# Kernel optimization log

Hardware: AMD Instinct MI355X
Metric: run time of the kernel (lower is better)

## Reference

```python
import jax, jax.numpy as jnp
import numpy as np

B, N, D, H = 8, 4096, 256, 4
KP, KN = N // 16, N // 32
EPS = 1e-6

def _ln(x, g, b):
    m = jnp.mean(x, -1, keepdims=True)
    v = jnp.var(x, -1, keepdims=True)
    return (x - m) / jnp.sqrt(v + 1e-5) * g + b

def _cross_attn(q_in, kv_in, wq, wk, wv, wo, bo):
    # q_in [1,Nq,D], kv_in [1,Nk,D]
    Bq, Nq, Dm = q_in.shape
    Nk = kv_in.shape[1]
    dh = Dm // H
    q = (q_in @ wq).reshape(Bq, Nq, H, dh).transpose(0, 2, 1, 3)
    k = (kv_in @ wk).reshape(Bq, Nk, H, dh).transpose(0, 2, 1, 3)
    v = (kv_in @ wv).reshape(Bq, Nk, H, dh).transpose(0, 2, 1, 3)
    attn = jax.nn.softmax(jnp.einsum('bhqd,bhkd->bhqk', q, k) * (dh ** -0.5), axis=-1)
    out = jnp.einsum('bhqk,bhkd->bhqd', attn, v).transpose(0, 2, 1, 3).reshape(Bq, Nq, Dm)
    return out @ wo + bo

def setup_inputs():
    key = jax.random.key(0)
    ks = jax.random.split(key, 40)
    f32 = jnp.float32
    def w(i, shape, s):
        return s * jax.random.normal(ks[i], shape, f32)
    inp = {}
    inp['x'] = jax.random.normal(ks[0], (B, N, D), f32)
    inp['mask'] = (jax.random.randint(ks[1], (B, N), 0, 3) - 1).astype(jnp.int32)  # values in {-1,0,1}
    inp['pos_emb'] = 0.02 * jax.random.normal(ks[2], (1, N, D), f32)
    inp['sim_p_w'] = w(3, (D, D), 0.2); inp['sim_p_b'] = jnp.zeros((D,), f32)
    inp['sim_n_w'] = w(4, (D, D), 0.2); inp['sim_n_b'] = jnp.zeros((D,), f32)
    inp['adj_w'] = w(5, (D, D), 0.05)
    inp['gnn_p_w1'] = w(6, (D, D), 0.05); inp['gnn_p_w2'] = w(7, (D, D), 0.05)
    inp['gnn_n_w1'] = w(8, (D, D), 0.05); inp['gnn_n_w2'] = w(9, (D, D), 0.05)
    for i in range(1, 6):
        inp['ln%d_g' % i] = jnp.ones((D,), f32)
        inp['ln%d_b' % i] = jnp.zeros((D,), f32)
    names = ['i2q_wq', 'i2q_wk', 'i2q_wv', 'i2q_wo', 'q2i_wq', 'q2i_wk', 'q2i_wv', 'q2i_wo']
    for j, nme in enumerate(names):
        inp[nme] = w(10 + j, (D, D), 0.05)
    inp['i2q_bo'] = jnp.zeros((D,), f32)
    inp['q2i_bo'] = jnp.zeros((D,), f32)
    inp['mlp_w'] = w(20, (D, D), 0.05); inp['mlp_b'] = jnp.zeros((D,), f32)
    inp['g_i2t'] = 0.1 * jax.random.normal(ks[21], (1, 1, D), f32)
    inp['g_t2i'] = 0.1 * jax.random.normal(ks[22], (1, 1, D), f32)
    return inp

def reference(x, mask, pos_emb, sim_p_w, sim_p_b, sim_n_w, sim_n_b, adj_w,
              gnn_p_w1, gnn_p_w2, gnn_n_w1, gnn_n_w2,
              ln1_g, ln1_b, ln2_g, ln2_b, ln3_g, ln3_b, ln4_g, ln4_b, ln5_g, ln5_b,
              i2q_wq, i2q_wk, i2q_wv, i2q_wo, i2q_bo,
              q2i_wq, q2i_wk, q2i_wv, q2i_wo, q2i_bo,
              mlp_w, mlp_b, g_i2t, g_t2i):
    pos_mask = (mask == 1).astype(x.dtype)[..., None]    # [B,N,1]
    neg_mask = (mask == -1).astype(x.dtype)[..., None]
    pos_query = (x * pos_mask).sum(1, keepdims=True) / (pos_mask.sum(1, keepdims=True) + EPS)  # [B,1,D]
    neg_query = (x * neg_mask).sum(1, keepdims=True) / (neg_mask.sum(1, keepdims=True) + EPS)
    pos_sim = jax.nn.sigmoid(((x @ sim_p_w + sim_p_b) * pos_query).sum(-1))  # [B,N]
    neg_sim = jax.nn.sigmoid(((x @ sim_n_w + sim_n_b) * neg_query).sum(-1))
    weight_p, idx_p = jax.lax.top_k(pos_sim, KP)
    weight_n, idx_n = jax.lax.top_k(neg_sim, KN)
    scale = 1.0 / jnp.sqrt(jnp.asarray(D, x.dtype))

    def gcn(node, w1, w2):
        adj = jax.nn.softmax((node @ adj_w) @ node.T * scale, axis=-1)  # [K,K]
        h = jax.nn.relu(adj @ (node @ w1))
        return adj @ (h @ w2)

    def batch_forward(ip, wp, inn, wn, feat):
        node_p = feat[ip] * (wp > 0.6).astype(feat.dtype)[:, None]       # [KP,D]
        query_p = gcn(node_p, gnn_p_w1, gnn_p_w2) + pos_emb[0, ip]
        node_n = feat[inn] * (wn > 0.6).astype(feat.dtype)[:, None]      # [KN,D]
        query_n = gcn(node_n, gnn_n_w1, gnn_n_w2) + pos_emb[0, inn]
        query = jnp.concatenate([query_p, query_n], 0)[None]             # [1,KP+KN,D]
        featb = feat[None]                                               # [1,N,D]
        query = query + g_i2t * _cross_attn(_ln(query, ln1_g, ln1_b), _ln(featb, ln2_g, ln2_b),
                                            i2q_wq, i2q_wk, i2q_wv, i2q_wo, i2q_bo)
        featb = featb + g_t2i * _cross_attn(_ln(featb, ln3_g, ln3_b), _ln(query, ln4_g, ln4_b),
                                            q2i_wq, q2i_wk, q2i_wv, q2i_wo, q2i_bo)
        featb = featb + (_ln(featb, ln5_g, ln5_b) @ mlp_w + mlp_b)
        return featb

    out = jax.vmap(batch_forward)(idx_p, weight_p, idx_n, weight_n, x)   # [B,1,N,D]
    return out, pos_sim, neg_sim
```

## Files before the change

### kernel.cpp

```cpp
#include <hip/hip_runtime.h>

#define BB 8
#define NN 4096
#define DD 256
#define HH 4
#define DHH 64
#define KPP 256
#define KNN 128
#define SCH 64

typedef float f32x4 __attribute__((ext_vector_type(4)));
typedef short bf16x8 __attribute__((ext_vector_type(8)));
typedef short bf16x4 __attribute__((ext_vector_type(4)));

#define FLAG_TRANSB 1
#define FLAG_RELU   2

__device__ __forceinline__ float bf2f(unsigned short u){
  union { unsigned int i; float f; } v; v.i = ((unsigned int)u) << 16; return v.f;
}
__device__ __forceinline__ unsigned short f2bf(float f){
  union { float f; unsigned int i; } v; v.f = f;
  return (unsigned short)((v.i + 0x7FFFu + ((v.i >> 16) & 1u)) >> 16);
}
// ... 8 lines not shown
                                                  float* __restrict__ pcnt){
  int b = blockIdx.y, c = blockIdx.x, t = threadIdx.x;
  int w = t >> 6, lane = t & 63;
  const int R = NN / SCH;
  int n0 = c * R;
  const float* xb = x + ((long)b*NN + n0)*DD;
  const int* mb = mask + (long)b*NN + n0;
  float4 sp = {0.f,0.f,0.f,0.f}, sn = {0.f,0.f,0.f,0.f};
  int cp = 0, cn = 0;
  #pragma unroll 4
  for (int r = w; r < R; r += 4){
    int mv = mb[r];
    float4 v = ((const float4*)(xb + (long)r*DD))[lane];
    if (mv == 1){ sp.x += v.x; sp.y += v.y; sp.z += v.z; sp.w += v.w; cp++; }
    else if (mv == -1){ sn.x += v.x; sn.y += v.y; sn.z += v.z; sn.w += v.w; cn++; }
  }
  __shared__ float red[2][4][256];
  __shared__ int cnt[2][4];
  ((float4*)&red[0][w][0])[lane] = sp;
  ((float4*)&red[1][w][0])[lane] = sn;
  if (lane == 0){ cnt[0][w] = cp; cnt[1][w] = cn; }
  __syncthreads();
  float s0 = red[0][0][t]+red[0][1][t]+red[0][2][t]+red[0][3][t];
  float s1 = red[1][0][t]+red[1][1][t]+red[1][2][t]+red[1][3][t];
  part[(((long)(b*SCH+c)*2+0)*DD)+t] = s0;
  part[(((long)(b*SCH+c)*2+1)*DD)+t] = s1;
  if (t == 0){
    pcnt[(b*SCH+c)*2+0] = (float)(cnt[0][0]+cnt[0][1]+cnt[0][2]+cnt[0][3]);
    pcnt[(b*SCH+c)*2+1] = (float)(cnt[1][0]+cnt[1][1]+cnt[1][2]+cnt[1][3]);
  }
}

__global__ void stats_vec(const float* __restrict__ part, const float* __restrict__ pcnt,
                          const float* __restrict__ Wp, const float* __restrict__ bp,
                          const float* __restrict__ Wn, const float* __restrict__ bn,
                          float* __restrict__ vvec, float* __restrict__ cscal){
  int b = blockIdx.x, k = threadIdx.x;
  __shared__ float qp[256], qn[256], red[256];
  {
    float sp=0.f, sn=0.f, cp=0.f, cn=0.f;
    for (int c = 0; c < SCH; c++){
      sp += part[(((long)(b*SCH+c)*2+0)*DD)+k];
      sn += part[(((long)(b*SCH+c)*2+1)*DD)+k];
      cp += pcnt[(b*SCH+c)*2+0];
      cn += pcnt[(b*SCH+c)*2+1];
    }
    qp[k] = sp / (cp + 1e-6f);
    qn[k] = sn / (cn + 1e-6f);
  }
  __syncthreads();
  float vp = 0.f, vn = 0.f;
  for (int j = 0; j < DD; j++){ vp += Wp[(long)k*DD+j]*qp[j]; vn += Wn[(long)k*DD+j]*qn[j]; }
  vvec[(long)(b*2+0)*DD+k] = vp; vvec[(long)(b*2+1)*DD+k] = vn;
  red[k] = bp[k]*qp[k];
  __syncthreads();
  for (int s = 128; s > 0; s >>= 1){ if (k < s) red[k] += red[k+s]; __syncthreads(); }
  if (k == 0) cscal[b*2+0] = red[0];
  __syncthreads();
  red[k] = bn[k]*qn[k];
  __syncthreads();
  for (int s = 128; s > 0; s >>= 1){ if (k < s) red[k] += red[k+s]; __syncthreads(); }
  if (k == 0) cscal[b*2+1] = red[0];
}

__global__ void sim_norm_kernel(const float* __restrict__ x, const float* __restrict__ vvec,
                                const float* __restrict__ cscal,
                                float* __restrict__ simP, float* __restrict__ simN,
                                unsigned short* __restrict__ xhat){
  int b = blockIdx.y;
  int w = threadIdx.x >> 6, lane = threadIdx.x & 63;
  int n = blockIdx.x*4 + w;
  long row = (long)b*NN + n;
  const float4* xr = (const float4*)(x + row*DD);
  float4 xv = xr[lane];
  float4 a = ((const float4*)(vvec + (long)(b*2+0)*DD))[lane];
  float4 c = ((const float4*)(vvec + (long)(b*2+1)*DD))[lane];
  float sp = xv.x*a.x + xv.y*a.y + xv.z*a.z + xv.w*a.w;
  float sn = xv.x*c.x + xv.y*c.y + xv.z*c.z + xv.w*c.w;
  float s  = xv.x+xv.y+xv.z+xv.w;
  float q  = xv.x*xv.x+xv.y*xv.y+xv.z*xv.z+xv.w*xv.w;
  for (int off = 32; off; off >>= 1){
    sp += __shfl_xor(sp, off); sn += __shfl_xor(sn, off);
    s  += __shfl_xor(s, off);  q  += __shfl_xor(q, off);
  }
  float m = s*(1.f/256.f);
  float var = q*(1.f/256.f) - m*m;
  float rinv = rsqrtf(var + 1e-5f);
  ushort4 o;
  o.x = f2bf((xv.x-m)*rinv); o.y = f2bf((xv.y-m)*rinv);
  o.z = f2bf((xv.z-m)*rinv); o.w = f2bf((xv.w-m)*rinv);
  ((ushort4*)(xhat + row*DD))[lane] = o;
  if (lane == 0){
    float zp = sp + cscal[b*2+0], zn = sn + cscal[b*2+1];
    simP[row] = 1.f/(1.f+expf(-zp));
    simN[row] = 1.f/(1.f+expf(-zn));
// ... 126 lines not shown
  float* a = A + (long)b*bs + (long)r*L;
  int e = L >> 6;
  float vals[4]; float mx = -1e30f;
  for (int j = 0; j < e; j++){ vals[j] = a[lane*e+j]; mx = fmaxf(mx, vals[j]); }
  for (int off = 32; off; off >>= 1) mx = fmaxf(mx, __shfl_xor(mx, off));
  float sum = 0.f;
  for (int j = 0; j < e; j++){ vals[j] = expf(vals[j]-mx); sum += vals[j]; }
  for (int off = 32; off; off >>= 1) sum += __shfl_xor(sum, off);
  float rinv = 1.f/sum;
  for (int j = 0; j < e; j++) a[lane*e+j] = vals[j]*rinv;
}

__global__ void rownorm_kernel(const float* __restrict__ X, unsigned short* __restrict__ Y, int rows){
  int w = threadIdx.x >> 6, lane = threadIdx.x & 63;
  long row = (long)blockIdx.x*4 + w;
  if (row >= rows) return;
  const float4* xr = (const float4*)(X + row*DD);
  float4 xv = xr[lane];
  float s = xv.x+xv.y+xv.z+xv.w;
  float q = xv.x*xv.x+xv.y*xv.y+xv.z*xv.z+xv.w*xv.w;
  for (int off = 32; off; off >>= 1){ s += __shfl_xor(s, off); q += __shfl_xor(q, off); }
  float m = s*(1.f/256.f);
  float var = q*(1.f/256.f) - m*m;
  float rinv = rsqrtf(var + 1e-5f);
  ushort4 o;
  o.x = f2bf((xv.x-m)*rinv); o.y = f2bf((xv.y-m)*rinv);
  o.z = f2bf((xv.z-m)*rinv); o.w = f2bf((xv.w-m)*rinv);
  ((ushort4*)(Y + row*DD))[lane] = o;
}

struct FoldArgs { const float* W[9]; const float* g[9]; unsigned short* BT[9]; float sc[9]; };
struct BiasArgs { const float* W[7]; const float* b[7]; const float* addb[7]; float* out[7]; float sc[7]; };

__global__ void fold_w(FoldArgs fa){
  int m = blockIdx.y, tile = blockIdx.x, t = threadIdx.x;
  const float* W = fa.W[m]; const float* g = fa.g[m]; unsigned short* BT = fa.BT[m];
  float sc = fa.sc[m];
  __shared__ float T[64][65];
  int tn = (tile & 3)*64, tk = (tile >> 2)*64;
  #pragma unroll 4
  for (int p = 0; p < 16; p++){
    int kl = p*4 + (t >> 6), nl = t & 63;
    float v = W[(long)(tk+kl)*256 + tn + nl];
    if (g) v *= g[tk+kl];
    T[kl][nl] = v * sc;
  }
  __syncthreads();
  #pragma unroll 4
  for (int p = 0; p < 16; p++){
    int nl = p*4 + (t >> 6), kl = t & 63;
    BT[(long)(tn+nl)*256 + tk + kl] = f2bf(T[kl][nl]);
  }
}

__global__ void fold_b(BiasArgs ba){
  int m = blockIdx.x, n = threadIdx.x;
  const float* W = ba.W[m]; const float* b = ba.b[m];
  float s = (ba.addb[m] != nullptr) ? ba.addb[m][n] : 0.f;
  for (int k = 0; k < 256; k++) s += b[k]*W[(long)k*256+n];
  ba.out[m][n] = s * ba.sc[m];
}

struct GP {
  const float* A; long sAb; int lda;
  const float* B; long sBb; int ldb;
  float* C; long sCb; int ldc;
  const int* pidx; const float* pe;
  int M, N, K; float alpha; int flags;
};
struct GP4 { GP p[4]; };

__global__ __launch_bounds__(256) void gemm_multi(GP4 g4){
  GP p = g4.p[blockIdx.z >> 3];
  int b = blockIdx.z & 7;
  int m0 = blockIdx.y*64, n0 = blockIdx.x*64;
  if (m0 >= p.M || n0 >= p.N) return;
  __shared__ __align__(16) unsigned short As[64*40];
  __shared__ __align__(16) unsigned short Bs[64*40];
  const float* Ab = p.A + (long)b*p.sAb;
  const float* Bb = p.B + (long)b*p.sBb;
  int t = threadIdx.x;
  int w = t >> 6, lane = t & 63, lrowi = lane & 15, lquad = lane >> 4;
  int wm = w >> 1, wn = w & 1;
  f32x4 acc[2][2];
  #pragma unroll
  for (int i = 0; i < 2; i++)
    #pragma unroll
    for (int j = 0; j < 2; j++) acc[i][j] = (f32x4){0.f,0.f,0.f,0.f};
  int am = t >> 2, akq = t & 3;
  for (int k0 = 0; k0 < p.K; k0 += 32){
    {
      const float4* s4 = (const float4*)(Ab + (long)(m0+am)*p.lda + k0 + akq*8);
      float4 u = s4[0], vv = s4[1];
// ... 21 lines not shown
    for (int i = 0; i < 2; i++)
      af[i] = *(const bf16x8*)(&As[(wm*32 + i*16 + lrowi)*40 + lquad*8]);
    #pragma unroll
    for (int j = 0; j < 2; j++)
      bfr[j] = *(const bf16x8*)(&Bs[(wn*32 + j*16 + lrowi)*40 + lquad*8]);
    #pragma unroll
    for (int i = 0; i < 2; i++)
      #pragma unroll
      for (int j = 0; j < 2; j++)
        acc[i][j] = __builtin_amdgcn_mfma_f32_16x16x32_bf16(af[i], bfr[j], acc[i][j], 0, 0, 0);
    __syncthreads();
  }
  float* Cb = p.C + (long)b*p.sCb;
  #pragma unroll
  for (int i = 0; i < 2; i++)
    #pragma unroll
    for (int j = 0; j < 2; j++){
      int col = n0 + wn*32 + j*16 + lrowi;
      #pragma unroll
      for (int r = 0; r < 4; r++){
        int row = m0 + wm*32 + i*16 + lquad*4 + r;
        float v = p.alpha*acc[i][j][r];
        if (p.flags & FLAG_RELU) v = fmaxf(v, 0.f);
        if (p.pidx != nullptr){
          int idx = p.pidx[b*512 + row];
          v += p.pe[(long)idx*256 + col];
        }
        Cb[(long)row*p.ldc + col] = v;
      }
    }
}

template<typename OT, bool RES, bool GATE>
__global__ __launch_bounds__(256) void gemm128(
    const unsigned short* __restrict__ A, long sAb,
    const unsigned short* __restrict__ BT,
    OT* __restrict__ C, long sCb, int ldc,
    const float* __restrict__ R, long sRb,
    const float* __restrict__ bias, const float* __restrict__ gate)
{
  __shared__ __align__(16) unsigned short As[2][4096];
  __shared__ __align__(16) unsigned short Bs[2][4096];
  int t = threadIdx.x;
  int w = t >> 6, lane = t & 63, lrowi = lane & 15, lquad = lane >> 4;
  int wm = w >> 1, wn = w & 1;
  int m0 = blockIdx.y*128, n0 = blockIdx.x*128;
  const unsigned short* Ab = A + (long)blockIdx.z*sAb + (long)m0*256;
  const unsigned short* Bb = BT + (long)n0*256;
  int g0 = t, g1 = 256 + t;
  int row0 = g0 >> 2, kq0 = g0 & 3;
  int row1 = g1 >> 2, kq1 = g1 & 3;
  f32x4 acc[4][4];
  #pragma unroll
  for (int i = 0; i < 4; i++)
    #pragma unroll
    for (int j = 0; j < 4; j++) acc[i][j] = (f32x4){0.f,0.f,0.f,0.f};

  auto stage = [&](int buf, int k0){
    gload16(Ab + (long)row0*256 + k0 + kq0*8, &As[buf][g0*8]);
    gload16(Ab + (long)row1*256 + k0 + kq1*8, &As[buf][g1*8]);
    gload16(Bb + (long)row0*256 + k0 + kq0*8, &Bs[buf][g0*8]);
    gload16(Bb + (long)row1*256 + k0 + kq1*8, &Bs[buf][g1*8]);
  };

  stage(0, 0);
  for (int it = 0; it < 8; it++){
    int cur = it & 1;
    if (it < 7){
      stage(cur ^ 1, (it+1)*32);
      __asm__ volatile("s_waitcnt vmcnt(4)" ::: "memory");
    } else {
      __asm__ volatile("s_waitcnt vmcnt(0)" ::: "memory");
    }
    __builtin_amdgcn_s_barrier();
    bf16x8 af[4], bfr[4];
    #pragma unroll
    for (int i = 0; i < 4; i++)
      af[i] = *(const bf16x8*)(&As[cur][((wm*64 + i*16 + lrowi)*4 + lquad)*8]);
    #pragma unroll
    for (int j = 0; j < 4; j++)
      bfr[j] = *(const bf16x8*)(&Bs[cur][((wn*64 + j*16 + lrowi)*4 + lquad)*8]);
    #pragma unroll
    for (int i = 0; i < 4; i++)
      #pragma unroll
      for (int j = 0; j < 4; j++)
        acc[i][j] = __builtin_amdgcn_mfma_f32_16x16x32_bf16(af[i], bfr[j], acc[i][j], 0, 0, 0);
    __asm__ volatile("s_waitcnt lgkmcnt(0)" ::: "memory");
    __builtin_amdgcn_s_barrier();
  }
  OT* Cb = C + (long)blockIdx.z*sCb;
  const float* Rb = RES ? (R + (long)blockIdx.z*sRb) : nullptr;
  #pragma unroll
  for (int j = 0; j < 4; j++){
    int col = n0 + wn*64 + j*16 + lrowi;
    float bv = bias[col];
    float gv = GATE ? gate[col] : 1.f;
    #pragma unroll
    for (int i = 0; i < 4; i++){
      #pragma unroll
      for (int r = 0; r < 4; r++){
        int row = m0 + wm*64 + i*16 + lquad*4 + r;
        float v = acc[i][j][r] + bv;
        if (GATE) v *= gv;
        if (RES) v += Rb[(long)row*256 + col];
        if constexpr (sizeof(OT) == 4) Cb[(long)row*ldc + col] = v;
        else                           Cb[(long)row*ldc + col] = f2bf(v);
      }
    }
  }
}

template<int NFRAG>
__global__ __launch_bounds__(256) void flash_kernel(
    const unsigned short* __restrict__ Q, long sQb, int ldq,
    const unsigned short* __restrict__ Kt, const unsigned short* __restrict__ Vt,
    long sKb, int ldkv,
    unsigned short* __restrict__ O, long sOb,
    float* __restrict__ Opart, float* __restrict__ Lpart,
    int Nq, int Nk, int nsplit)
{
  __shared__ __align__(16) unsigned short Kl[32*72];
  __shared__ __align__(16) unsigned short Vl[64*36];
  __shared__ __align__(16) unsigned short Pl[4*NFRAG*16*36];
  int b = blockIdx.z, h = blockIdx.y;
  int nqg = Nq / (64*NFRAG);
  int qg = blockIdx.x % nqg, split = blockIdx.x / nqg;
  int kchunk = Nk / nsplit;
  int kbeg = split*kchunk, kend = kbeg + kchunk;
  int t = threadIdx.x, w = t >> 6, lane = t & 63, lrowi = lane & 15, lquad = lane >> 4;
  int q0 = qg*(64*NFRAG) + w*(16*NFRAG);
  const unsigned short* Qb = Q + (long)b*sQb + h*DHH;
  const unsigned short* Kb = Kt + (long)b*sKb + h*DHH;
  const unsigned short* Vb = Vt + (long)b*sKb + h*DHH;
  bf16x8 qa[NFRAG][2];
  #pragma unroll
  for (int f = 0; f < NFRAG; f++)
    #pragma unroll
    for (int kt = 0; kt < 2; kt++)
      qa[f][kt] = *(const bf16x8*)(Qb + (long)(q0 + f*16 + lrowi)*ldq + kt*32 + lquad*8);

  f32x4 o[NFRAG][4];
  float psum[NFRAG][4];
  #pragma unroll
  for (int f = 0; f < NFRAG; f++)
    #pragma unroll
    for (int cj = 0; cj < 4; cj++){
      o[f][cj] = (f32x4){0.f,0.f,0.f,0.f};
      psum[f][cj] = 0.f;
    }
  int skq = t >> 3, sdq = (t & 7)*8;
  int skrow = ((skq & 1) << 4) | (skq >> 1);
  int vkq = t & 31, vdq = (t >> 5)*8;
  unsigned short* Pw = &Pl[w*(NFRAG*16*36)];

  for (int kt0 = kbeg; kt0 < kend; kt0 += 32){
    {
      uint4 kv = *(const uint4*)(Kb + (long)(kt0+skq)*ldkv + sdq);
      *(uint4*)(&Kl[skrow*72 + sdq]) = kv;
      uint4 vv = *(const uint4*)(Vb + (long)(kt0+vkq)*ldkv + vdq);
      const unsigned short* vp = (const unsigned short*)&vv;
      #pragma unroll
      for (int j = 0; j < 8; j++) Vl[(vdq+j)*36 + vkq] = vp[j];
    }
    __syncthreads();
    bf16x8 kb0 = *(const bf16x8*)(&Kl[(0*16+lrowi)*72 + lquad*8]);
    bf16x8 kb1 = *(const bf16x8*)(&Kl[(0*16+lrowi)*72 + 32 + lquad*8]);
    bf16x8 kb2 = *(const bf16x8*)(&Kl[(1*16+lrowi)*72 + lquad*8]);
    bf16x8 kb3 = *(const bf16x8*)(&Kl[(1*16+lrowi)*72 + 32 + lquad*8]);
    union { bf16x8 v8; bf16x4 v4[2]; } vbu[4];
    #pragma unroll
    for (int cj = 0; cj < 4; cj++){
      const unsigned short* vb = &Vl[(cj*16+lrowi)*36 + lquad*8];
      vbu[cj].v4[0] = *(const bf16x4*)vb;
      vbu[cj].v4[1] = *(const bf16x4*)(vb + 4);
    }
    #pragma unroll
    for (int f = 0; f < NFRAG; f++){
      f32x4 S0 = (f32x4){0.f,0.f,0.f,0.f}, S1 = (f32x4){0.f,0.f,0.f,0.f};
      __builtin_amdgcn_s_setprio(1);
      S0 = __builtin_amdgcn_mfma_f32_16x16x32_bf16(qa[f][0], kb0, S0, 0, 0, 0);
      S0 = __builtin_amdgcn_mfma_f32_16x16x32_bf16(qa[f][1], kb1, S0, 0, 0, 0);
      S1 = __builtin_amdgcn_mfma_f32_16x16x32_bf16(qa[f][0], kb2, S1, 0, 0, 0);
      S1 = __builtin_amdgcn_mfma_f32_16x16x32_bf16(qa[f][1], kb3, S1, 0, 0, 0);
      __builtin_amdgcn_s_setprio(0);
      unsigned short* Pf = Pw + f*(16*36);
      #pragma unroll
      for (int r = 0; r < 4; r++){
        float p0 = exp2f(S0[r]);
        float p1 = exp2f(S1[r]);
        psum[f][r] += p0 + p1;
        unsigned int pk;
        asm("v_cvt_pk_bf16_f32 %0, %1, %2" : "=v"(pk) : "v"(p0), "v"(p1));
        *(unsigned int*)(&Pf[(lquad*4+r)*36 + 2*lrowi]) = pk;
      }
    }
    __asm__ volatile("s_waitcnt lgkmcnt(0)" ::: "memory");
    #pragma unroll
    for (int f = 0; f < NFRAG; f++){
      const unsigned short* pp = &Pw[f*(16*36) + lrowi*36 + lquad*8];
      union { bf16x8 v8; bf16x4 v4[2]; } pa;
      pa.v4[0] = *(const bf16x4*)pp;
      pa.v4[1] = *(const bf16x4*)(pp + 4);
      __builtin_amdgcn_s_setprio(1);
      #pragma unroll
      for (int cj = 0; cj < 4; cj++)
        o[f][cj] = __builtin_amdgcn_mfma_f32_16x16x32_bf16(pa.v8, vbu[cj].v8, o[f][cj], 0, 0, 0);
      __builtin_amdgcn_s_setprio(0);
    }
    __syncthreads();
  }
  float lsum[NFRAG][4];
  #pragma unroll
  for (int f = 0; f < NFRAG; f++)
    #pragma unroll
    for (int r = 0; r < 4; r++){
      float s = psum[f][r];
      #pragma unroll
      for (int off = 1; off < 16; off <<= 1) s += __shfl_xor(s, off);
      lsum[f][r] = s;
    }
  if (nsplit > 1){
    int p = (b*HH + h)*nsplit + split;
    float* Op = Opart + (long)p*Nq*DHH;
    #pragma unroll
    for (int f = 0; f < NFRAG; f++)
      #pragma unroll
      for (int r = 0; r < 4; r++){
        int row = q0 + f*16 + lquad*4 + r;
        #pragma unroll
        for (int cj = 0; cj < 4; cj++)
          Op[(long)row*DHH + cj*16 + lrowi] = o[f][cj][r];
        if (lrowi == 0) Lpart[(long)p*Nq + row] = lsum[f][r];
      }
  } else {
    unsigned short* Ob = O + (long)b*sOb + h*DHH;
    #pragma unroll
    for (int f = 0; f < NFRAG; f++)
      #pragma unroll
      for (int r = 0; r < 4; r++){
        float rl = 1.f/lsum[f][r];
// ... 40 lines not shown
  const float* ln2_g = (const float*)d_in[14]; const float* ln2_b = (const float*)d_in[15];
  const float* ln3_g = (const float*)d_in[16]; const float* ln3_b = (const float*)d_in[17];
  const float* ln4_g = (const float*)d_in[18]; const float* ln4_b = (const float*)d_in[19];
  const float* ln5_g = (const float*)d_in[20]; const float* ln5_b = (const float*)d_in[21];
  const float* i2q_wq = (const float*)d_in[22];
  const float* i2q_wk = (const float*)d_in[23];
  const float* i2q_wv = (const float*)d_in[24];
  const float* i2q_wo = (const float*)d_in[25];
  const float* q2i_wq = (const float*)d_in[26];
  const float* q2i_wk = (const float*)d_in[27];
  const float* q2i_wv = (const float*)d_in[28];
  const float* q2i_wo = (const float*)d_in[29];
  const float* i2q_bo = (const float*)d_in[30];
  const float* q2i_bo = (const float*)d_in[31];
  const float* mlp_w  = (const float*)d_in[32];
  const float* mlp_b  = (const float*)d_in[33];
  const float* g_i2t  = (const float*)d_in[34];
  const float* g_t2i  = (const float*)d_in[35];

  float* out  = (float*)d_out;
  float* simP = out + (size_t)BB*NN*DD;
  float* simN = simP + (size_t)BB*NN;

  char* w8 = (char*)d_ws;
  size_t off = 0;
  auto take = [&](size_t bytes)->void*{
    void* p = (void*)(w8 + off);
    off += (bytes + 255) & ~(size_t)255;
    return p;
  };
  float* part   = (float*)take((size_t)BB*SCH*2*DD*4);
  float* pcnt   = (float*)take((size_t)BB*SCH*2*4);
  float* vvec   = (float*)take((size_t)BB*2*DD*4);
  float* cscal  = (float*)take((size_t)BB*2*4);
  int*   idxb   = (int*)take((size_t)BB*2*256*4);
  float* wb     = (float*)take((size_t)BB*2*256*4);
  float* node   = (float*)take((size_t)BB*384*DD*4);
  float* gA     = (float*)take((size_t)BB*384*DD*4);
  float* gadjP  = (float*)take((size_t)BB*256*256*4);
  float* gadjN  = (float*)take((size_t)BB*128*128*4);
  float* query  = (float*)take((size_t)BB*384*DD*4);
  float* query2 = (float*)take((size_t)BB*384*DD*4);
  unsigned short* xhatq  = (unsigned short*)take((size_t)BB*384*DD*2);
  unsigned short* qh     = (unsigned short*)take((size_t)BB*384*DD*2);
  unsigned short* attnZ  = (unsigned short*)take((size_t)BB*384*DD*2);
  unsigned short* xhatq2 = (unsigned short*)take((size_t)BB*384*DD*2);
  unsigned short* kv2    = (unsigned short*)take((size_t)BB*384*512*2);
  unsigned short* xhat   = (unsigned short*)take((size_t)BB*NN*DD*2);
  unsigned short* kvq    = (unsigned short*)take((size_t)BB*NN*768*2);
  float* featb2 = (float*)take((size_t)BB*NN*DD*4);
  float* Lpart  = (float*)take((size_t)BB*HH*8*384*4);
  unsigned short* wTq1  = (unsigned short*)take((size_t)65536*2);
  unsigned short* wTbig = (unsigned short*)take((size_t)3*65536*2);
  unsigned short* wTkv2 = (unsigned short*)take((size_t)2*65536*2);
  unsigned short* wTmlp = (unsigned short*)take((size_t)65536*2);
  unsigned short* wTo1  = (unsigned short*)take((size_t)65536*2);
  unsigned short* wTo2  = (unsigned short*)take((size_t)65536*2);
  float* biasQ1  = (float*)take(256*4);
  float* biasBig = (float*)take(768*4);
  float* biasKV2 = (float*)take(512*4);
  float* biasMlp = (float*)take(256*4);
  float* t1 = query;
  float* t2 = query2;
  float* t3 = gA;
  unsigned short* attn2 = xhat;
  unsigned short* xhat5 = kvq;
  float* Opart = featb2;

  const long sQ  = 384L*DD;
  const long sX  = (long)NN*DD;
  const float* NF = nullptr;

  const float QS = 0.125f * 1.44269504088896f;

  FoldArgs fa;
  fa.W[0]=i2q_wq; fa.g[0]=ln1_g; fa.BT[0]=wTq1;            fa.sc[0]=QS;
  fa.W[1]=i2q_wk; fa.g[1]=ln2_g; fa.BT[1]=wTbig;           fa.sc[1]=1.f;
  fa.W[2]=i2q_wv; fa.g[2]=ln2_g; fa.BT[2]=wTbig + 256*256; fa.sc[2]=1.f;
  fa.W[3]=q2i_wq; fa.g[3]=ln3_g; fa.BT[3]=wTbig + 512*256; fa.sc[3]=QS;
  fa.W[4]=q2i_wk; fa.g[4]=ln4_g; fa.BT[4]=wTkv2;           fa.sc[4]=1.f;
  fa.W[5]=q2i_wv; fa.g[5]=ln4_g; fa.BT[5]=wTkv2 + 256*256; fa.sc[5]=1.f;
  fa.W[6]=mlp_w;  fa.g[6]=ln5_g; fa.BT[6]=wTmlp;           fa.sc[6]=1.f;
  fa.W[7]=i2q_wo; fa.g[7]=nullptr; fa.BT[7]=wTo1;          fa.sc[7]=1.f;
  fa.W[8]=q2i_wo; fa.g[8]=nullptr; fa.BT[8]=wTo2;          fa.sc[8]=1.f;
  fold_w<<<dim3(16,9), 256, 0, stream>>>(fa);
  BiasArgs ba;
  ba.W[0]=i2q_wq; ba.b[0]=ln1_b; ba.addb[0]=nullptr; ba.out[0]=biasQ1;     ba.sc[0]=QS;
  ba.W[1]=i2q_wk; ba.b[1]=ln2_b; ba.addb[1]=nullptr; ba.out[1]=biasBig;    ba.sc[1]=1.f;
  ba.W[2]=i2q_wv; ba.b[2]=ln2_b; ba.addb[2]=nullptr; ba.out[2]=biasBig+256; ba.sc[2]=1.f;
  ba.W[3]=q2i_wq; ba.b[3]=ln3_b; ba.addb[3]=nullptr; ba.out[3]=biasBig+512; ba.sc[3]=QS;
  ba.W[4]=q2i_wk; ba.b[4]=ln4_b; ba.addb[4]=nullptr; ba.out[4]=biasKV2;    ba.sc[4]=1.f;
  ba.W[5]=q2i_wv; ba.b[5]=ln4_b; ba.addb[5]=nullptr; ba.out[5]=biasKV2+256; ba.sc[5]=1.f;
  ba.W[6]=mlp_w;  ba.b[6]=ln5_b; ba.addb[6]=mlp_b;   ba.out[6]=biasMlp;    ba.sc[6]=1.f;
  fold_b<<<7, 256, 0, stream>>>(ba);

  stats_part<<<dim3(SCH, BB), 256, 0, stream>>>(x, mask, part, pcnt);
  stats_vec<<<BB, 256, 0, stream>>>(part, pcnt, sim_p_w, sim_p_b, sim_n_w, sim_n_b, vvec, cscal);
  sim_norm_kernel<<<dim3(NN/4, BB), 256, 0, stream>>>(x, vvec, cscal, simP, simN, xhat);
  topk_radix<<<2*BB, 256, 0, stream>>>(simP, simN, x, idxb, wb, node);

  GP z = {};
  {
    GP4 g;
    g.p[0] = { node, 384L*DD, 256, adj_w, 0, 256, gA, 384L*DD, 256, nullptr, nullptr, 384, 256, 256, 1.f, 0 };
    g.p[1] = { node, 384L*DD, 256, gnn_p_w1, 0, 256, t1, 384L*DD, 256, nullptr, nullptr, 256, 256, 256, 1.f, 0 };
    g.p[2] = { node + 256L*DD, 384L*DD, 256, gnn_n_w1, 0, 256, t1 + 256L*DD, 384L*DD, 256, nullptr, nullptr, 128, 256, 256, 1.f, 0 };
    g.p[3] = z;
    gemm_multi<<<dim3(4,6,3*BB), 256, 0, stream>>>(g);
  }
  {
    GP4 g;
    g.p[0] = { gA, 384L*DD, 256, node, 384L*DD, 256, gadjP, 65536L, 256, nullptr, nullptr, 256, 256, 256, 0.0625f, FLAG_TRANSB };
    g.p[1] = { gA + 256L*DD, 384L*DD, 256, node + 256L*DD, 384L*DD, 256, gadjN, 16384L, 128, nullptr, nullptr, 128, 128, 256, 0.0625f, FLAG_TRANSB };
    g.p[2] = z; g.p[3] = z;
    gemm_multi<<<dim3(4,4,2*BB), 256, 0, stream>>>(g);
  }
  softmax_dual<<<768, 256, 0, stream>>>(gadjP, 256, 256, 65536L, BB*256,
                                        gadjN, 128, 128, 16384L, BB*128);
  {
    GP4 g;
    g.p[0] = { gadjP, 65536L, 256, t1, 384L*DD, 256, t2, 384L*DD, 256, nullptr, nullptr, 256, 256, 256, 1.f, FLAG_RELU };
    g.p[1] = { gadjN, 16384L, 128, t1 + 256L*DD, 384L*DD, 256, t2 + 256L*DD, 384L*DD, 256, nullptr, nullptr, 128, 256, 128, 1.f, FLAG_RELU };
    g.p[2] = z; g.p[3] = z;
    gemm_multi<<<dim3(4,4,2*BB), 256, 0, stream>>>(g);
  }
  {
    GP4 g;
    g.p[0] = { t2, 384L*DD, 256, gnn_p_w2, 0, 256, t3, 384L*DD, 256, nullptr, nullptr, 256, 256, 256, 1.f, 0 };
    g.p[1] = { t2 + 256L*DD, 384L*DD, 256, gnn_n_w2, 0, 256, t3 + 256L*DD, 384L*DD, 256, nullptr, nullptr, 128, 256, 256, 1.f, 0 };
    g.p[2] = z; g.p[3] = z;
    gemm_multi<<<dim3(4,4,2*BB), 256, 0, stream>>>(g);
  }
  {
    GP4 g;
    g.p[0] = { gadjP, 65536L, 256, t3, 384L*DD, 256, query, 384L*DD, 256, idxb, pos_emb, 256, 256, 256, 1.f, 0 };
    g.p[1] = { gadjN, 16384L, 128, t3 + 256L*DD, 384L*DD, 256, query + 256L*DD, 384L*DD, 256, idxb + 256, pos_emb, 128, 256, 128, 1.f, 0 };
    g.p[2] = z; g.p[3] = z;
    gemm_multi<<<dim3(4,4,2*BB), 256, 0, stream>>>(g);
  }

  rownorm_kernel<<<BB*384/4, 256, 0, stream>>>(query, xhatq, BB*384);

  gemm128<unsigned short,false,false><<<dim3(2,3,BB),256,0,stream>>>(
      xhatq, sQ, wTq1, qh, sQ, 256, NF, 0, biasQ1, NF);
  gemm128<unsigned short,false,false><<<dim3(6,32,BB),256,0,stream>>>(
      xhat, sX, wTbig, kvq, (long)NN*768, 768, NF, 0, biasBig, NF);
  flash_kernel<3><<<dim3(2*8, HH, BB), 256, 0, stream>>>(
      qh, sQ, 256, kvq, kvq + 256, (long)NN*768, 768,
      attnZ, sQ, Opart, Lpart, 384, NN, 8);
  flash_combine<<<BB*HH*384/4, 256, 0, stream>>>(Opart, Lpart, attnZ, sQ, 384, 8);
  gemm128<float,true,true><<<dim3(2,3,BB),256,0,stream>>>(
      attnZ, sQ, wTo1, query2, sQ, 256, query, sQ, i2q_bo, g_i2t);

  rownorm_kernel<<<BB*384/4, 256, 0, stream>>>(query2, xhatq2, BB*384);
  gemm128<unsigned short,false,false><<<dim3(4,3,BB),256,0,stream>>>(
      xhatq2, sQ, wTkv2, kv2, 384L*512, 512, NF, 0, biasKV2, NF);
  flash_kernel<2><<<dim3(32, HH, BB), 256, 0, stream>>>(
      kvq + 512, (long)NN*768, 768, kv2, kv2 + 256, 384L*512, 512,
      attn2, sX, nullptr, nullptr, NN, 384, 1);
  gemm128<float,true,true><<<dim3(2,32,BB),256,0,stream>>>(
      attn2, sX, wTo2, featb2, sX, 256, x, sX, q2i_bo, g_t2i);

  rownorm_kernel<<<BB*NN/4, 256, 0, stream>>>(featb2, xhat5, BB*NN);
  gemm128<float,true,false><<<dim3(2,32,BB),256,0,stream>>>(
      xhat5, sX, wTmlp, out, sX, 256, featb2, sX, biasMlp, NF);
}
```

Before: 477.0 us.

## Merge fold and pair GEMM launches, parallelize sim vector, unroll flash K loop

Merges the weight-fold and bias-fold kernels into one launch. Moves the per-batch sim-vector matvec out of an 8-block kernel into a separate kernel with 64 blocks. Fuses the Q-projection GEMM and the big KV GEMM into a single launch. Makes the flash kernel load two 32-key K/V tiles per barrier to halve synchronisation. These changes cut launch overhead and serial latency in small kernels, at the cost of more shared memory and registers in the flash kernel.

```diff
diff --git a/kernel.cpp b/kernel.cpp
--- a/kernel.cpp
+++ b/kernel.cpp
@@ -64,35 +64,53 @@
 }
 
 __global__ void stats_vec(const float* __restrict__ part, const float* __restrict__ pcnt,
-                          const float* __restrict__ Wp, const float* __restrict__ bp,
-                          const float* __restrict__ Wn, const float* __restrict__ bn,
-                          float* __restrict__ vvec, float* __restrict__ cscal){
+                          const float* __restrict__ bp, const float* __restrict__ bn,
+                          float* __restrict__ qpn, float* __restrict__ cscal){
   int b = blockIdx.x, k = threadIdx.x;
-  __shared__ float qp[256], qn[256], red[256];
-  {
-    float sp=0.f, sn=0.f, cp=0.f, cn=0.f;
-    for (int c = 0; c < SCH; c++){
-      sp += part[(((long)(b*SCH+c)*2+0)*DD)+k];
-      sn += part[(((long)(b*SCH+c)*2+1)*DD)+k];
-      cp += pcnt[(b*SCH+c)*2+0];
-      cn += pcnt[(b*SCH+c)*2+1];
-    }
-    qp[k] = sp / (cp + 1e-6f);
-    qn[k] = sn / (cn + 1e-6f);
-  }
-  __syncthreads();
-  float vp = 0.f, vn = 0.f;
-  for (int j = 0; j < DD; j++){ vp += Wp[(long)k*DD+j]*qp[j]; vn += Wn[(long)k*DD+j]*qn[j]; }
-  vvec[(long)(b*2+0)*DD+k] = vp; vvec[(long)(b*2+1)*DD+k] = vn;
-  red[k] = bp[k]*qp[k];
+  __shared__ float red[256];
+  float sp=0.f, sn=0.f, cp=0.f, cn=0.f;
+  for (int c = 0; c < SCH; c++){
+    sp += part[(((long)(b*SCH+c)*2+0)*DD)+k];
+    sn += part[(((long)(b*SCH+c)*2+1)*DD)+k];
+    cp += pcnt[(b*SCH+c)*2+0];
+    cn += pcnt[(b*SCH+c)*2+1];
+  }
+  float qpv = sp / (cp + 1e-6f);
+  float qnv = sn / (cn + 1e-6f);
+  qpn[(long)(b*2+0)*DD + k] = qpv;
+  qpn[(long)(b*2+1)*DD + k] = qnv;
+  red[k] = bp[k]*qpv;
   __syncthreads();
   for (int s = 128; s > 0; s >>= 1){ if (k < s) red[k] += red[k+s]; __syncthreads(); }
   if (k == 0) cscal[b*2+0] = red[0];
   __syncthreads();
-  red[k] = bn[k]*qn[k];
+  red[k] = bn[k]*qnv;
   __syncthreads();
   for (int s = 128; s > 0; s >>= 1){ if (k < s) red[k] += red[k+s]; __syncthreads(); }
   if (k == 0) cscal[b*2+1] = red[0];
+}
+
+__global__ void simvec_par(const float* __restrict__ qpn,
+                           const float* __restrict__ Wp, const float* __restrict__ Wn,
+                           float* __restrict__ vvec){
+  int c = blockIdx.x, b = blockIdx.y, t = threadIdx.x;
+  __shared__ float qp[256], qn[256];
+  qp[t] = qpn[(long)(b*2+0)*DD + t];
+  qn[t] = qpn[(long)(b*2+1)*DD + t];
+  __syncthreads();
+  int row = c*32 + (t >> 3);
+  int seg = (t & 7)*32;
+  const float* wp = Wp + (long)row*DD + seg;
+  const float* wn = Wn + (long)row*DD + seg;
+  float ap = 0.f, an = 0.f;
+  #pragma unroll 8
+  for (int j = 0; j < 32; j++){ ap += wp[j]*qp[seg+j]; an += wn[j]*qn[seg+j]; }
+  #pragma unroll
+  for (int off = 1; off < 8; off <<= 1){ ap += __shfl_xor(ap, off); an += __shfl_xor(an, off); }
+  if ((t & 7) == 0){
+    vvec[(long)(b*2+0)*DD + row] = ap;
+    vvec[(long)(b*2+1)*DD + row] = an;
+  }
 }
 
 __global__ void sim_norm_kernel(const float* __restrict__ x, const float* __restrict__ vvec,
@@ -285,33 +303,34 @@
 struct FoldArgs { const float* W[9]; const float* g[9]; unsigned short* BT[9]; float sc[9]; };
 struct BiasArgs { const float* W[7]; const float* b[7]; const float* addb[7]; float* out[7]; float sc[7]; };
 
-__global__ void fold_w(FoldArgs fa){
-  int m = blockIdx.y, tile = blockIdx.x, t = threadIdx.x;
-  const float* W = fa.W[m]; const float* g = fa.g[m]; unsigned short* BT = fa.BT[m];
-  float sc = fa.sc[m];
+__global__ void fold_all(FoldArgs fa, BiasArgs ba){
   __shared__ float T[64][65];
-  int tn = (tile & 3)*64, tk = (tile >> 2)*64;
-  #pragma unroll 4
-  for (int p = 0; p < 16; p++){
-    int kl = p*4 + (t >> 6), nl = t & 63;
-    float v = W[(long)(tk+kl)*256 + tn + nl];
-    if (g) v *= g[tk+kl];
-    T[kl][nl] = v * sc;
-  }
-  __syncthreads();
-  #pragma unroll 4
-  for (int p = 0; p < 16; p++){
-    int nl = p*4 + (t >> 6), kl = t & 63;
-    BT[(long)(tn+nl)*256 + tk + kl] = f2bf(T[kl][nl]);
-  }
-}
-
-__global__ void fold_b(BiasArgs ba){
-  int m = blockIdx.x, n = threadIdx.x;
-  const float* W = ba.W[m]; const float* b = ba.b[m];
-  float s = (ba.addb[m] != nullptr) ? ba.addb[m][n] : 0.f;
-  for (int k = 0; k < 256; k++) s += b[k]*W[(long)k*256+n];
-  ba.out[m][n] = s * ba.sc[m];
+  int t = threadIdx.x;
+  if (blockIdx.y < 9){
+    int m = blockIdx.y, tile = blockIdx.x;
+    const float* W = fa.W[m]; const float* g = fa.g[m]; unsigned short* BT = fa.BT[m];
+    float sc = fa.sc[m];
+    int tn = (tile & 3)*64, tk = (tile >> 2)*64;
+    #pragma unroll 4
+    for (int p = 0; p < 16; p++){
+      int kl = p*4 + (t >> 6), nl = t & 63;
+      float v = W[(long)(tk+kl)*256 + tn + nl];
+      if (g) v *= g[tk+kl];
+      T[kl][nl] = v * sc;
+    }
+    __syncthreads();
+    #pragma unroll 4
+    for (int p = 0; p < 16; p++){
+      int nl = p*4 + (t >> 6), kl = t & 63;
+      BT[(long)(tn+nl)*256 + tk + kl] = f2bf(T[kl][nl]);
+    }
+  } else if (blockIdx.x < 7){
+    int m = blockIdx.x, n = t;
+    const float* W = ba.W[m]; const float* b = ba.b[m];
+    float s = (ba.addb[m] != nullptr) ? ba.addb[m][n] : 0.f;
+    for (int k = 0; k < 256; k++) s += b[k]*W[(long)k*256+n];
+    ba.out[m][n] = s * ba.sc[m];
+  }
 }
 
 struct GP {
@@ -399,6 +418,85 @@
 }
 
 template<typename OT, bool RES, bool GATE>
+__device__ __forceinline__ void gemm128_body(
+    const unsigned short* __restrict__ A, long sAb,
+    const unsigned short* __restrict__ BT,
+    OT* __restrict__ C, long sCb, int ldc,
+    const float* __restrict__ R, long sRb,
+    const float* __restrict__ bias, const float* __restrict__ gate,
+    int bx, int by, int bz,
+    unsigned short (&As)[2][4096], unsigned short (&Bs)[2][4096])
+{
+  int t = threadIdx.x;
+  int w = t >> 6, lane = t & 63, lrowi = lane & 15, lquad = lane >> 4;
+  int wm = w >> 1, wn = w & 1;
+  int m0 = by*128, n0 = bx*128;
+  const unsigned short* Ab = A + (long)bz*sAb + (long)m0*256;
+  const unsigned short* Bb = BT + (long)n0*256;
+  int g0 = t, g1 = 256 + t;
+  int row0 = g0 >> 2, kq0 = g0 & 3;
+  int row1 = g1 >> 2, kq1 = g1 & 3;
+  f32x4 acc[4][4];
+  #pragma unroll
+  for (int i = 0; i < 4; i++)
+    #pragma unroll
+    for (int j = 0; j < 4; j++) acc[i][j] = (f32x4){0.f,0.f,0.f,0.f};
+
+  auto stage = [&](int buf, int k0){
+    gload16(Ab + (long)row0*256 + k0 + kq0*8, &As[buf][g0*8]);
+    gload16(Ab + (long)row1*256 + k0 + kq1*8, &As[buf][g1*8]);
+    gload16(Bb + (long)row0*256 + k0 + kq0*8, &Bs[buf][g0*8]);
+    gload16(Bb + (long)row1*256 + k0 + kq1*8, &Bs[buf][g1*8]);
+  };
+
+  stage(0, 0);
+  for (int it = 0; it < 8; it++){
+    int cur = it & 1;
+    if (it < 7){
+      stage(cur ^ 1, (it+1)*32);
+      __asm__ volatile("s_waitcnt vmcnt(4)" ::: "memory");
+    } else {
+      __asm__ volatile("s_waitcnt vmcnt(0)" ::: "memory");
+    }
+    __builtin_amdgcn_s_barrier();
+    bf16x8 af[4], bfr[4];
+    #pragma unroll
+    for (int i = 0; i < 4; i++)
+      af[i] = *(const bf16x8*)(&As[cur][((wm*64 + i*16 + lrowi)*4 + lquad)*8]);
+    #pragma unroll
+    for (int j = 0; j < 4; j++)
+      bfr[j] = *(const bf16x8*)(&Bs[cur][((wn*64 + j*16 + lrowi)*4 + lquad)*8]);
+    #pragma unroll
+    for (int i = 0; i < 4; i++)
+      #pragma unroll
+      for (int j = 0; j < 4; j++)
+        acc[i][j] = __builtin_amdgcn_mfma_f32_16x16x32_bf16(af[i], bfr[j], acc[i][j], 0, 0, 0);
+    __asm__ volatile("s_waitcnt lgkmcnt(0)" ::: "memory");
+    __builtin_amdgcn_s_barrier();
+  }
+  OT* Cb = C + (long)bz*sCb;
+  const float* Rb = RES ? (R + (long)bz*sRb) : nullptr;
+  #pragma unroll
+  for (int j = 0; j < 4; j++){
+    int col = n0 + wn*64 + j*16 + lrowi;
+    float bv = bias[col];
+    float gv = GATE ? gate[col] : 1.f;
+    #pragma unroll
+    for (int i = 0; i < 4; i++){
+      #pragma unroll
+      for (int r = 0; r < 4; r++){
+        int row = m0 + wm*64 + i*16 + lquad*4 + r;
+        float v = acc[i][j][r] + bv;
+        if (GATE) v *= gv;
+        if (RES) v += Rb[(long)row*256 + col];
+        if constexpr (sizeof(OT) == 4) Cb[(long)row*ldc + col] = v;
+        else                           Cb[(long)row*ldc + col] = f2bf(v);
+      }
+    }
+  }
+}
+
+template<typename OT, bool RES, bool GATE>
 __global__ __launch_bounds__(256) void gemm128(
     const unsigned short* __restrict__ A, long sAb,
     const unsigned short* __restrict__ BT,
@@ -408,72 +506,26 @@
 {
   __shared__ __align__(16) unsigned short As[2][4096];
   __shared__ __align__(16) unsigned short Bs[2][4096];
-  int t = threadIdx.x;
-  int w = t >> 6, lane = t & 63, lrowi = lane & 15, lquad = lane >> 4;
-  int wm = w >> 1, wn = w & 1;
-  int m0 = blockIdx.y*128, n0 = blockIdx.x*128;
-  const unsigned short* Ab = A + (long)blockIdx.z*sAb + (long)m0*256;
-  const unsigned short* Bb = BT + (long)n0*256;
-  int g0 = t, g1 = 256 + t;
-  int row0 = g0 >> 2, kq0 = g0 & 3;
-  int row1 = g1 >> 2, kq1 = g1 & 3;
-  f32x4 acc[4][4];
-  #pragma unroll
-  for (int i = 0; i < 4; i++)
-    #pragma unroll
-    for (int j = 0; j < 4; j++) acc[i][j] = (f32x4){0.f,0.f,0.f,0.f};
-
-  auto stage = [&](int buf, int k0){
-    gload16(Ab + (long)row0*256 + k0 + kq0*8, &As[buf][g0*8]);
-    gload16(Ab + (long)row1*256 + k0 + kq1*8, &As[buf][g1*8]);
-    gload16(Bb + (long)row0*256 + k0 + kq0*8, &Bs[buf][g0*8]);
-    gload16(Bb + (long)row1*256 + k0 + kq1*8, &Bs[buf][g1*8]);
-  };
-
-  stage(0, 0);
-  for (int it = 0; it < 8; it++){
-    int cur = it & 1;
-    if (it < 7){
-      stage(cur ^ 1, (it+1)*32);
-      __asm__ volatile("s_waitcnt vmcnt(4)" ::: "memory");
-    } else {
-      __asm__ volatile("s_waitcnt vmcnt(0)" ::: "memory");
-    }
-    __builtin_amdgcn_s_barrier();
-    bf16x8 af[4], bfr[4];
-    #pragma unroll
-    for (int i = 0; i < 4; i++)
-      af[i] = *(const bf16x8*)(&As[cur][((wm*64 + i*16 + lrowi)*4 + lquad)*8]);
-    #pragma unroll
-    for (int j = 0; j < 4; j++)
-      bfr[j] = *(const bf16x8*)(&Bs[cur][((wn*64 + j*16 + lrowi)*4 + lquad)*8]);
-    #pragma unroll
-    for (int i = 0; i < 4; i++)
-      #pragma unroll
-      for (int j = 0; j < 4; j++)
-        acc[i][j] = __builtin_amdgcn_mfma_f32_16x16x32_bf16(af[i], bfr[j], acc[i][j], 0, 0, 0);
-    __asm__ volatile("s_waitcnt lgkmcnt(0)" ::: "memory");
-    __builtin_amdgcn_s_barrier();
-  }
-  OT* Cb = C + (long)blockIdx.z*sCb;
-  const float* Rb = RES ? (R + (long)blockIdx.z*sRb) : nullptr;
-  #pragma unroll
-  for (int j = 0; j < 4; j++){
-    int col = n0 + wn*64 + j*16 + lrowi;
-    float bv = bias[col];
-    float gv = GATE ? gate[col] : 1.f;
-    #pragma unroll
-    for (int i = 0; i < 4; i++){
-      #pragma unroll
-      for (int r = 0; r < 4; r++){
-        int row = m0 + wm*64 + i*16 + lquad*4 + r;
-        float v = acc[i][j][r] + bv;
-        if (GATE) v *= gv;
-        if (RES) v += Rb[(long)row*256 + col];
-        if constexpr (sizeof(OT) == 4) Cb[(long)row*ldc + col] = v;
-        else                           Cb[(long)row*ldc + col] = f2bf(v);
-      }
-    }
+  gemm128_body<OT,RES,GATE>(A, sAb, BT, C, sCb, ldc, R, sRb, bias, gate,
+                            blockIdx.x, blockIdx.y, blockIdx.z, As, Bs);
+}
+
+__global__ __launch_bounds__(256) void gemm128_pair(
+    const unsigned short* __restrict__ A0, long sA0, const unsigned short* __restrict__ B0,
+    unsigned short* __restrict__ C0, long sC0, int ldc0, const float* __restrict__ bias0,
+    const unsigned short* __restrict__ A1, long sA1, const unsigned short* __restrict__ B1,
+    unsigned short* __restrict__ C1, long sC1, int ldc1, const float* __restrict__ bias1)
+{
+  __shared__ __align__(16) unsigned short As[2][4096];
+  __shared__ __align__(16) unsigned short Bs[2][4096];
+  int x = blockIdx.x, z = blockIdx.z;
+  if (x < 192){
+    gemm128_body<unsigned short,false,false>(A0, sA0, B0, C0, sC0, ldc0, nullptr, 0, bias0, nullptr,
+                                             x % 6, x / 6, z, As, Bs);
+  } else {
+    int xx = x - 192;
+    gemm128_body<unsigned short,false,false>(A1, sA1, B1, C1, sC1, ldc1, nullptr, 0, bias1, nullptr,
+                                             xx % 2, xx / 2, z, As, Bs);
   }
 }
 
@@ -486,8 +538,8 @@
     float* __restrict__ Opart, float* __restrict__ Lpart,
     int Nq, int Nk, int nsplit)
 {
-  __shared__ __align__(16) unsigned short Kl[32*72];
-  __shared__ __align__(16) unsigned short Vl[64*36];
+  __shared__ __align__(16) unsigned short Kl[2][32*72];
+  __shared__ __align__(16) unsigned short Vl[2][64*36];
   __shared__ __align__(16) unsigned short Pl[4*NFRAG*16*36];
   int b = blockIdx.z, h = blockIdx.y;
   int nqg = Nq / (64*NFRAG);
@@ -520,59 +572,68 @@
   int vkq = t & 31, vdq = (t >> 5)*8;
   unsigned short* Pw = &Pl[w*(NFRAG*16*36)];
 
-  for (int kt0 = kbeg; kt0 < kend; kt0 += 32){
+  for (int kt0 = kbeg; kt0 < kend; kt0 += 64){
     {
-      uint4 kv = *(const uint4*)(Kb + (long)(kt0+skq)*ldkv + sdq);
-      *(uint4*)(&Kl[skrow*72 + sdq]) = kv;
-      uint4 vv = *(const uint4*)(Vb + (long)(kt0+vkq)*ldkv + vdq);
-      const unsigned short* vp = (const unsigned short*)&vv;
-      #pragma unroll
-      for (int j = 0; j < 8; j++) Vl[(vdq+j)*36 + vkq] = vp[j];
+      uint4 k0v = *(const uint4*)(Kb + (long)(kt0+skq)*ldkv + sdq);
+      uint4 v0v = *(const uint4*)(Vb + (long)(kt0+vkq)*ldkv + vdq);
+      uint4 k1v = *(const uint4*)(Kb + (long)(kt0+32+skq)*ldkv + sdq);
+      uint4 v1v = *(const uint4*)(Vb + (long)(kt0+32+vkq)*ldkv + vdq);
+      *(uint4*)(&Kl[0][skrow*72 + sdq]) = k0v;
+      const unsigned short* vp0 = (const unsigned short*)&v0v;
+      #pragma unroll
+      for (int j = 0; j < 8; j++) Vl[0][(vdq+j)*36 + vkq] = vp0[j];
+      *(uint4*)(&Kl[1][skrow*72 + sdq]) = k1v;
+      const unsigned short* vp1 = (const unsigned short*)&v1v;
+      #pragma unroll
+      for (int j = 0; j < 8; j++) Vl[1][(vdq+j)*36 + vkq] = vp1[j];
     }
     __syncthreads();
-    bf16x8 kb0 = *(const bf16x8*)(&Kl[(0*16+lrowi)*72 + lquad*8]);
-    bf16x8 kb1 = *(const bf16x8*)(&Kl[(0*16+lrowi)*72 + 32 + lquad*8]);
-    bf16x8 kb2 = *(const bf16x8*)(&Kl[(1*16+lrowi)*72 + lquad*8]);
-    bf16x8 kb3 = *(const bf16x8*)(&Kl[(1*16+lrowi)*72 + 32 + lquad*8]);
-    union { bf16x8 v8; bf16x4 v4[2]; } vbu[4];
-    #pragma unroll
-    for (int cj = 0; cj < 4; cj++){
-      const unsigned short* vb = &Vl[(cj*16+lrowi)*36 + lquad*8];
-      vbu[cj].v4[0] = *(const bf16x4*)vb;
-      vbu[cj].v4[1] = *(const bf16x4*)(vb + 4);
-    }
-    #pragma unroll
-    for (int f = 0; f < NFRAG; f++){
-      f32x4 S0 = (f32x4){0.f,0.f,0.f,0.f}, S1 = (f32x4){0.f,0.f,0.f,0.f};
-      __builtin_amdgcn_s_setprio(1);
-      S0 = __builtin_amdgcn_mfma_f32_16x16x32_bf16(qa[f][0], kb0, S0, 0, 0, 0);
-      S0 = __builtin_amdgcn_mfma_f32_16x16x32_bf16(qa[f][1], kb1, S0, 0, 0, 0);
-      S1 = __builtin_amdgcn_mfma_f32_16x16x32_bf16(qa[f][0], kb2, S1, 0, 0, 0);
-      S1 = __builtin_amdgcn_mfma_f32_16x16x32_bf16(qa[f][1], kb3, S1, 0, 0, 0);
-      __builtin_amdgcn_s_setprio(0);
-      unsigned short* Pf = Pw + f*(16*36);
-      #pragma unroll
-      for (int r = 0; r < 4; r++){
-        float p0 = exp2f(S0[r]);
-        float p1 = exp2f(S1[r]);
-        psum[f][r] += p0 + p1;
-        unsigned int pk;
-        asm("v_cvt_pk_bf16_f32 %0, %1, %2" : "=v"(pk) : "v"(p0), "v"(p1));
-        *(unsigned int*)(&Pf[(lquad*4+r)*36 + 2*lrowi]) = pk;
+    #pragma unroll
+    for (int s = 0; s < 2; s++){
+      bf16x8 kb0 = *(const bf16x8*)(&Kl[s][(0*16+lrowi)*72 + lquad*8]);
+      bf16x8 kb1 = *(const bf16x8*)(&Kl[s][(0*16+lrowi)*72 + 32 + lquad*8]);
+      bf16x8 kb2 = *(const bf16x8*)(&Kl[s][(1*16+lrowi)*72 + lquad*8]);
+      bf16x8 kb3 = *(const bf16x8*)(&Kl[s][(1*16+lrowi)*72 + 32 + lquad*8]);
+      union { bf16x8 v8; bf16x4 v4[2]; } vbu[4];
+      #pragma unroll
+      for (int cj = 0; cj < 4; cj++){
+        const unsigned short* vb = &Vl[s][(cj*16+lrowi)*36 + lquad*8];
+        vbu[cj].v4[0] = *(const bf16x4*)vb;
+        vbu[cj].v4[1] = *(const bf16x4*)(vb + 4);
       }
-    }
-    __asm__ volatile("s_waitcnt lgkmcnt(0)" ::: "memory");
-    #pragma unroll
-    for (int f = 0; f < NFRAG; f++){
-      const unsigned short* pp = &Pw[f*(16*36) + lrowi*36 + lquad*8];
-      union { bf16x8 v8; bf16x4 v4[2]; } pa;
-      pa.v4[0] = *(const bf16x4*)pp;
-      pa.v4[1] = *(const bf16x4*)(pp + 4);
-      __builtin_amdgcn_s_setprio(1);
-      #pragma unroll
-      for (int cj = 0; cj < 4; cj++)
-        o[f][cj] = __builtin_amdgcn_mfma_f32_16x16x32_bf16(pa.v8, vbu[cj].v8, o[f][cj], 0, 0, 0);
-      __builtin_amdgcn_s_setprio(0);
+      #pragma unroll
+      for (int f = 0; f < NFRAG; f++){
+        f32x4 S0 = (f32x4){0.f,0.f,0.f,0.f}, S1 = (f32x4){0.f,0.f,0.f,0.f};
+        __builtin_amdgcn_s_setprio(1);
+        S0 = __builtin_amdgcn_mfma_f32_16x16x32_bf16(qa[f][0], kb0, S0, 0, 0, 0);
+        S0 = __builtin_amdgcn_mfma_f32_16x16x32_bf16(qa[f][1], kb1, S0, 0, 0, 0);
+        S1 = __builtin_amdgcn_mfma_f32_16x16x32_bf16(qa[f][0], kb2, S1, 0, 0, 0);
+        S1 = __builtin_amdgcn_mfma_f32_16x16x32_bf16(qa[f][1], kb3, S1, 0, 0, 0);
+        __builtin_amdgcn_s_setprio(0);
+        unsigned short* Pf = Pw + f*(16*36);
+        #pragma unroll
+        for (int r = 0; r < 4; r++){
+          float p0 = exp2f(S0[r]);
+          float p1 = exp2f(S1[r]);
+          psum[f][r] += p0 + p1;
+          unsigned int pk;
+          asm("v_cvt_pk_bf16_f32 %0, %1, %2" : "=v"(pk) : "v"(p0), "v"(p1));
+          *(unsigned int*)(&Pf[(lquad*4+r)*36 + 2*lrowi]) = pk;
+        }
+      }
+      __asm__ volatile("s_waitcnt lgkmcnt(0)" ::: "memory");
+      #pragma unroll
+      for (int f = 0; f < NFRAG; f++){
+        const unsigned short* pp = &Pw[f*(16*36) + lrowi*36 + lquad*8];
+        union { bf16x8 v8; bf16x4 v4[2]; } pa;
+        pa.v4[0] = *(const bf16x4*)pp;
+        pa.v4[1] = *(const bf16x4*)(pp + 4);
+        __builtin_amdgcn_s_setprio(1);
+        #pragma unroll
+        for (int cj = 0; cj < 4; cj++)
+          o[f][cj] = __builtin_amdgcn_mfma_f32_16x16x32_bf16(pa.v8, vbu[cj].v8, o[f][cj], 0, 0, 0);
+        __builtin_amdgcn_s_setprio(0);
+      }
     }
     __syncthreads();
   }
@@ -679,6 +740,7 @@
   float* part   = (float*)take((size_t)BB*SCH*2*DD*4);
   float* pcnt   = (float*)take((size_t)BB*SCH*2*4);
   float* vvec   = (float*)take((size_t)BB*2*DD*4);
+  float* qpn    = (float*)take((size_t)BB*2*DD*4);
   float* cscal  = (float*)take((size_t)BB*2*4);
   int*   idxb   = (int*)take((size_t)BB*2*256*4);
   float* wb     = (float*)take((size_t)BB*2*256*4);
@@ -730,7 +792,6 @@
   fa.W[6]=mlp_w;  fa.g[6]=ln5_g; fa.BT[6]=wTmlp;           fa.sc[6]=1.f;
   fa.W[7]=i2q_wo; fa.g[7]=nullptr; fa.BT[7]=wTo1;          fa.sc[7]=1.f;
   fa.W[8]=q2i_wo; fa.g[8]=nullptr; fa.BT[8]=wTo2;          fa.sc[8]=1.f;
-  fold_w<<<dim3(16,9), 256, 0, stream>>>(fa);
   BiasArgs ba;
   ba.W[0]=i2q_wq; ba.b[0]=ln1_b; ba.addb[0]=nullptr; ba.out[0]=biasQ1;     ba.sc[0]=QS;
   ba.W[1]=i2q_wk; ba.b[1]=ln2_b; ba.addb[1]=nullptr; ba.out[1]=biasBig;    ba.sc[1]=1.f;
@@ -739,10 +800,11 @@
   ba.W[4]=q2i_wk; ba.b[4]=ln4_b; ba.addb[4]=nullptr; ba.out[4]=biasKV2;    ba.sc[4]=1.f;
   ba.W[5]=q2i_wv; ba.b[5]=ln4_b; ba.addb[5]=nullptr; ba.out[5]=biasKV2+256; ba.sc[5]=1.f;
   ba.W[6]=mlp_w;  ba.b[6]=ln5_b; ba.addb[6]=mlp_b;   ba.out[6]=biasMlp;    ba.sc[6]=1.f;
-  fold_b<<<7, 256, 0, stream>>>(ba);
+  fold_all<<<dim3(16,10), 256, 0, stream>>>(fa, ba);
 
   stats_part<<<dim3(SCH, BB), 256, 0, stream>>>(x, mask, part, pcnt);
-  stats_vec<<<BB, 256, 0, stream>>>(part, pcnt, sim_p_w, sim_p_b, sim_n_w, sim_n_b, vvec, cscal);
+  stats_vec<<<BB, 256, 0, stream>>>(part, pcnt, sim_p_b, sim_n_b, qpn, cscal);
+  simvec_par<<<dim3(8, BB), 256, 0, stream>>>(qpn, sim_p_w, sim_n_w, vvec);
   sim_norm_kernel<<<dim3(NN/4, BB), 256, 0, stream>>>(x, vvec, cscal, simP, simN, xhat);
   topk_radix<<<2*BB, 256, 0, stream>>>(simP, simN, x, idxb, wb, node);
 
@@ -788,10 +850,9 @@
 
   rownorm_kernel<<<BB*384/4, 256, 0, stream>>>(query, xhatq, BB*384);
 
-  gemm128<unsigned short,false,false><<<dim3(2,3,BB),256,0,stream>>>(
-      xhatq, sQ, wTq1, qh, sQ, 256, NF, 0, biasQ1, NF);
-  gemm128<unsigned short,false,false><<<dim3(6,32,BB),256,0,stream>>>(
-      xhat, sX, wTbig, kvq, (long)NN*768, 768, NF, 0, biasBig, NF);
+  gemm128_pair<<<dim3(198,1,BB),256,0,stream>>>(
+      xhat, sX, wTbig, kvq, (long)NN*768, 768, biasBig,
+      xhatq, sQ, wTq1, qh, sQ, 256, biasQ1);
   flash_kernel<3><<<dim3(2*8, HH, BB), 256, 0, stream>>>(
       qh, sQ, 256, kvq, kvq + 256, (long)NN*768, 768,
       attnZ, sQ, Opart, Lpart, 384, NN, 8);
```

After: 456.0 us. 4.4% less time.
